# Kernel optimization log

Hardware: AMD Instinct MI355X
Metric: run time of the kernel (lower is better)

## Reference

```python
import jax, jax.numpy as jnp
import numpy as np

N_NODES = 100_000
N_EDGES = 3_200_000
F_IN, F_HID, F_OUT = 128, 128, 128
MLP_HID, MLP_OUT = 256, 64


def setup_inputs() -> dict:
    key = jax.random.key(0)
    ks = jax.random.split(key, 11)
    def w(k, shape):
        fan_in = shape[0]
        return jax.random.normal(k, shape, jnp.float32) / jnp.sqrt(jnp.float32(fan_in))
    return {
        'x':   jax.random.normal(ks[0], (N_NODES, F_IN), jnp.float32),
        'src': jax.random.randint(ks[1], (N_EDGES,), 0, N_NODES, jnp.int32),
        'dst': jax.random.randint(ks[2], (N_EDGES,), 0, N_NODES, jnp.int32),
        'w1':  w(ks[3], (F_IN, F_HID)),  'b1': jnp.zeros((F_HID,), jnp.float32),
        'w2':  w(ks[4], (F_HID, F_OUT)), 'b2': jnp.zeros((F_OUT,), jnp.float32),
        'wm1': w(ks[5], (F_OUT, MLP_HID)), 'bm1': jnp.zeros((MLP_HID,), jnp.float32),
        'wm2': w(ks[6], (MLP_HID, MLP_OUT)), 'bm2': jnp.zeros((MLP_OUT,), jnp.float32),
    }


def reference(x, src, dst, w1, b1, w2, b2, wm1, bm1, wm2, bm2):
    n = x.shape[0]
    ones = jnp.ones(src.shape[0], x.dtype)
    # DGL GraphConv norm='both': clamp degrees to >=1, symmetric D^-1/2 A D^-1/2
    out_norm = jnp.clip(jax.ops.segment_sum(ones, src, num_segments=n), 1.0) ** -0.5
    in_norm = jnp.clip(jax.ops.segment_sum(ones, dst, num_segments=n), 1.0) ** -0.5

    def gconv(h, w, b):
        msg = (h * out_norm[:, None])[src]                       # [E, F] gather
        agg = jax.ops.segment_sum(msg, dst, num_segments=n)      # [N, F] scatter-add
        return (agg * in_norm[:, None]) @ w + b

    h = jax.nn.relu(gconv(x, w1, b1))   # conv1 + relu (dropout is identity in eval)
    h = jax.nn.relu(gconv(h, w2, b2))   # conv2 + relu
    h = jax.nn.relu(h @ wm1 + bm1)      # MLP hidden layer
    return h @ wm2 + bm2                # MLP output (no final activation)
```

## Files before the change

### kernel.cpp

```cpp
#include <hip/hip_runtime.h>
#include <hip/hip_bf16.h>
#include <cstdint>

__device__ __forceinline__ unsigned short f2b(float f) {
    union { float f; unsigned int i; } v; v.f = f;
    unsigned int i = v.i;
    unsigned int r = (i + 0x7FFFu + ((i >> 16) & 1u)) >> 16;
    return (unsigned short)r;
}
__device__ __forceinline__ float b2f_lo(unsigned int p) {
    union { unsigned int i; float f; } v; v.i = p << 16; return v.f;
}
__device__ __forceinline__ float b2f_hi(unsigned int p) {
    union { unsigned int i; float f; } v; v.i = p & 0xFFFF0000u; return v.f;
}
__device__ __forceinline__ unsigned int pack2(float a, float b) {
    return (unsigned int)f2b(a) | ((unsigned int)f2b(b) << 16);
}

typedef __attribute__((__ext_vector_type__(8))) __bf16 bf16x8;
typedef __attribute__((__ext_vector_type__(4))) float  f32x4;

#define N_NODES 100000
#define N_EDGES 3200000
#define NBUCK   200
#define BSZ     500

__global__ void k_hist2(const int* __restrict__ src, const int* __restrict__ dst,
                        int* __restrict__ gcntA, int* __restrict__ gcntB, int E) {
    __shared__ int hA[NBUCK], hB[NBUCK];
    int t = threadIdx.x;
    if (t < NBUCK) { hA[t] = 0; hB[t] = 0; }
    __syncthreads();
    for (int i = blockIdx.x * blockDim.x + t; i < E; i += gridDim.x * blockDim.x) {
        atomicAdd(&hA[dst[i] / BSZ], 1);
        atomicAdd(&hB[src[i] / BSZ], 1);
    }
    __syncthreads();
    if (t < NBUCK) {
        if (hA[t]) atomicAdd(&gcntA[t], hA[t]);
        if (hB[t]) atomicAdd(&gcntB[t], hB[t]);
    }
}

__global__ void k_scan_coarse(const int* __restrict__ gcntA, const int* __restrict__ gcntB,
                              int* __restrict__ gbaseA, int* __restrict__ gbaseB,
                              int* __restrict__ gcurA, int* __restrict__ gcurB,
                              int* __restrict__ offsets) {
    __shared__ int pA[256], pB[256];
    int t = threadIdx.x;
    int vA = (t < NBUCK) ? gcntA[t] : 0;
    int vB = (t < NBUCK) ? gcntB[t] : 0;
    pA[t] = vA; pB[t] = vB;
    __syncthreads();
    for (int d = 1; d < 256; d <<= 1) {
        int a = (t >= d) ? pA[t - d] : 0;
        int b = (t >= d) ? pB[t - d] : 0;
        __syncthreads();
        pA[t] += a; pB[t] += b;
        __syncthreads();
    }
    if (t < NBUCK) {
        gbaseA[t] = pA[t] - vA; gcurA[t] = pA[t] - vA;
        gbaseB[t] = pB[t] - vB; gcurB[t] = pB[t] - vB;
    }
    if (t == 255) {
        gbaseA[NBUCK] = pA[255];
        gbaseB[NBUCK] = pB[255];
        offsets[N_NODES] = pA[255];
    }
}

__global__ void k_scatter(const int* __restrict__ src, const int* __restrict__ dst,
                          int* __restrict__ gcurA, int* __restrict__ gcurB,
                          unsigned* __restrict__ pairs, int* __restrict__ keysB, int E) {
    __shared__ int hA[NBUCK], hB[NBUCK], baA[NBUCK], baB[NBUCK], lcA[NBUCK], lcB[NBUCK];
    int t = threadIdx.x;
    const int CHUNK = 12500;
    int lo = blockIdx.x * CHUNK, hi = min(lo + CHUNK, E);
    if (t < NBUCK) { hA[t] = 0; hB[t] = 0; }
    __syncthreads();
    for (int i = lo + t; i < hi; i += 256) {
        atomicAdd(&hA[dst[i] / BSZ], 1);
        atomicAdd(&hB[src[i] / BSZ], 1);
    }
    __syncthreads();
    if (t < NBUCK) {
        baA[t] = hA[t] ? atomicAdd(&gcurA[t], hA[t]) : 0;
        lcA[t] = 0;
        baB[t] = hB[t] ? atomicAdd(&gcurB[t], hB[t]) : 0;
        lcB[t] = 0;
    }
    __syncthreads();
    for (int i = lo + t; i < hi; i += 256) {
        int s = src[i], d = dst[i];
        int bA = d / BSZ;
        int l  = atomicAdd(&lcA[bA], 1);
        pairs[baA[bA] + l] = ((unsigned)(d - bA * BSZ) << 17) | (unsigned)s;
        int bB = s / BSZ;
        int l2 = atomicAdd(&lcB[bB], 1);
        keysB[baB[bB] + l2] = s;
    }
}

__global__ void k_csr_bucket(const unsigned* __restrict__ pairs, const int* __restrict__ gbaseA,
                             int* __restrict__ offsets, float* __restrict__ in_norm,
                             int* __restrict__ esrc) {
    __shared__ int hist[512], scan[512], curs[512];
    int b = blockIdx.x, t = threadIdx.x;
    int node0 = b * BSZ;
    int bstart = gbaseA[b], bend = gbaseA[b + 1];
    if (t < 512) hist[t] = 0;
    __syncthreads();
    for (int i = bstart + t; i < bend; i += 1024)
        atomicAdd(&hist[pairs[i] >> 17], 1);
    __syncthreads();
    if (t < 512) scan[t] = hist[t];
    __syncthreads();
    for (int d = 1; d < 512; d <<= 1) {
        int v = (t < 512 && t >= d) ? scan[t - d] : 0;
        __syncthreads();
        if (t < 512) scan[t] += v;
        __syncthreads();
    }
    if (t < BSZ) {
        int excl = scan[t] - hist[t];
        offsets[node0 + t] = bstart + excl;
        in_norm[node0 + t] = rsqrtf((float)max(hist[t], 1));
        curs[t] = excl;
    }
    __syncthreads();
    for (int i = bstart + t; i < bend; i += 1024) {
        unsigned p = pairs[i];
        int d = (int)(p >> 17);
        int l = atomicAdd(&curs[d], 1);
        esrc[bstart + l] = (int)(p & 0x1FFFFu);
    }
}

__global__ void k_sortwave(const int* __restrict__ offsets, int* __restrict__ esrc, int N) {
    int node = blockIdx.x * 4 + (threadIdx.x >> 6);
    if (node >= N) return;
    int lane = threadIdx.x & 63;
    int lo = offsets[node], hi = offsets[node + 1];
    int len = hi - lo;
    if (len <= 1) return;
    const int INF = 0x7FFFFFFF;
    int v0 = (lane < len) ? esrc[lo + lane] : INF;
    int v1 = (64 + lane < len) ? esrc[lo + 64 + lane] : INF;
#pragma unroll
    for (int k = 2; k <= 128; k <<= 1) {
#pragma unroll
        for (int d = 64; d > 0; d >>= 1) {
            if (d >= k) continue;
            if (d == 64) {
                int a = min(v0, v1), b = max(v0, v1);
                v0 = a; v1 = b;
            } else {
                int w0 = __shfl_xor(v0, d, 64);
                int w1 = __shfl_xor(v1, d, 64);
                bool up0 = ((lane & k) == 0);
                bool up1 = (((64 + lane) & k) == 0);
                bool lower = ((lane & d) == 0);
                v0 = (lower == up0) ? min(v0, w0) : max(v0, w0);
                v1 = (lower == up1) ? min(v1, w1) : max(v1, w1);
            }
        }
    }
    if (lane < len) esrc[lo + lane] = v0;
    if (64 + lane < len) esrc[lo + 64 + lane] = v1;
}

__global__ void k_count_scale(const int* __restrict__ keys, const int* __restrict__ gbaseB,
                              const float4* __restrict__ x4, float* __restrict__ out_norm,
                              uint2* __restrict__ xs) {
    __shared__ int hist[512];
    __shared__ float onl[BSZ];
    int b = blockIdx.x, t = threadIdx.x;
    int node0 = b * BSZ;
    int bstart = gbaseB[b], bend = gbaseB[b + 1];
    if (t < 512) hist[t] = 0;
    __syncthreads();
    for (int i = bstart + t; i < bend; i += 1024)
        atomicAdd(&hist[keys[i] - node0], 1);
    __syncthreads();
    if (t < BSZ) {
        float on = rsqrtf((float)max(hist[t], 1));
        onl[t] = on;
        out_norm[node0 + t] = on;
    }
    __syncthreads();
    size_t base4 = (size_t)node0 * 32;
    for (int i = t; i < BSZ * 32; i += 1024) {
        float on = onl[i >> 5];
        float4 v = x4[base4 + i];
        uint2 o;
        o.x = pack2(v.x * on, v.y * on);
        o.y = pack2(v.z * on, v.w * on);
        xs[base4 + i] = o;
    }
}

__global__ void k_transpose4(const float* __restrict__ w1, const float* __restrict__ w2,
                             const float* __restrict__ wm1, const float* __restrict__ wm2,
                             unsigned short* __restrict__ t1, unsigned short* __restrict__ t2,
                             unsigned short* __restrict__ tm1, unsigned short* __restrict__ tm2) {
    int i = blockIdx.x * blockDim.x + threadIdx.x;
    const float* w; unsigned short* t; int N, idx;
    if (i < 16384)       { w = w1;  t = t1;  N = 128; idx = i; }
    else if (i < 32768)  { w = w2;  t = t2;  N = 128; idx = i - 16384; }
    else if (i < 65536)  { w = wm1; t = tm1; N = 256; idx = i - 32768; }
    else if (i < 81920)  { w = wm2; t = tm2; N = 64;  idx = i - 65536; }
    else return;
    int K = (i < 65536) ? 128 : 256;
    int k = idx / N, n = idx - k * N;
    t[(size_t)n * K + k] = f2b(w[idx]);
}

#define AGG_ADD(p)                                                              \
        a0 += b2f_lo(p.x); a1 += b2f_hi(p.x);                                   \
        a2 += b2f_lo(p.y); a3 += b2f_hi(p.y);                                   \
        a4 += b2f_lo(p.z); a5 += b2f_hi(p.z);                                   \
        a6 += b2f_lo(p.w); a7 += b2f_hi(p.w);

#define AGG_NODE_BODY(node)                                                     \
    int lo = offsets[node], hi = offsets[node + 1];                             \
    float a0 = 0.f, a1 = 0.f, a2 = 0.f, a3 = 0.f,                               \
          a4 = 0.f, a5 = 0.f, a6 = 0.f, a7 = 0.f;                               \
    int k = lo + g;                                                             \
    for (; k + 12 < hi; k += 16) {                                              \
        int s0 = esrc[k];                                                       \
        int s1 = esrc[k + 4];                                                   \
        int s2 = esrc[k + 8];                                                   \
        int s3 = esrc[k + 12];                                                  \
        uint4 p0 = feat[(size_t)s0 * 16 + c];                                   \
        uint4 p1 = feat[(size_t)s1 * 16 + c];                                   \
        uint4 p2 = feat[(size_t)s2 * 16 + c];                                   \
        uint4 p3 = feat[(size_t)s3 * 16 + c];                                   \
        AGG_ADD(p0) AGG_ADD(p1) AGG_ADD(p2) AGG_ADD(p3)                         \
    }                                                                           \
    for (; k < hi; k += 4) {                                                    \
        int s = esrc[k];                                                        \
        uint4 p = feat[(size_t)s * 16 + c];                                     \
        AGG_ADD(p)                                                              \
    }                                                                           \
    a0 += __shfl_xor(a0, 16, 64); a0 += __shfl_xor(a0, 32, 64);                 \
    a1 += __shfl_xor(a1, 16, 64); a1 += __shfl_xor(a1, 32, 64);                 \
    a2 += __shfl_xor(a2, 16, 64); a2 += __shfl_xor(a2, 32, 64);                 \
    a3 += __shfl_xor(a3, 16, 64); a3 += __shfl_xor(a3, 32, 64);                 \
    a4 += __shfl_xor(a4, 16, 64); a4 += __shfl_xor(a4, 32, 64);                 \
    a5 += __shfl_xor(a5, 16, 64); a5 += __shfl_xor(a5, 32, 64);                 \
    a6 += __shfl_xor(a6, 16, 64); a6 += __shfl_xor(a6, 32, 64);                 \
    a7 += __shfl_xor(a7, 16, 64); a7 += __shfl_xor(a7, 32, 64);

__global__ __launch_bounds__(256, 8)
void k_conv(const int* __restrict__ offsets, const int* __restrict__ esrc,
            const uint4* __restrict__ feat, const float* __restrict__ in_norm,
            const unsigned short* __restrict__ WT, const float* __restrict__ bias,
            const float* __restrict__ row_scale, unsigned short* __restrict__ C,
            int N) {
    __shared__ unsigned short A[32][136];
    int wv = threadIdx.x >> 6, lane = threadIdx.x & 63;
    int row0 = blockIdx.x * 32;
    int g = lane >> 4, c = lane & 15;

    for (int i = 0; i < 8; ++i) {
        int nl = wv * 8 + i;
        int node = row0 + nl;
        AGG_NODE_BODY(node)
        if (g == 0) {
            float inn = in_norm[node];
            uint4 o;
            o.x = pack2(a0 * inn, a1 * inn);
            o.y = pack2(a2 * inn, a3 * inn);
            o.z = pack2(a4 * inn, a5 * inn);
            o.w = pack2(a6 * inn, a7 * inn);
            *(uint4*)&A[nl][c * 8] = o;
        }
    }
    __syncthreads();

    int m = lane & 15, q = lane >> 4;
    const unsigned short* b0 = WT + (size_t)(wv * 32 + m) * 128 + q * 8;
    const unsigned short* b1 = b0 + (size_t)16 * 128;
    f32x4 acc00 = {0.f, 0.f, 0.f, 0.f}, acc10 = {0.f, 0.f, 0.f, 0.f};
    f32x4 acc01 = {0.f, 0.f, 0.f, 0.f}, acc11 = {0.f, 0.f, 0.f, 0.f};
#pragma unroll
    for (int k = 0; k < 128; k += 32) {
        bf16x8 bf0 = *(const bf16x8*)(b0 + k);
        bf16x8 bf1 = *(const bf16x8*)(b1 + k);
        bf16x8 af0 = *(const bf16x8*)&A[m][q * 8 + k];
        bf16x8 af1 = *(const bf16x8*)&A[16 + m][q * 8 + k];
        acc00 = __builtin_amdgcn_mfma_f32_16x16x32_bf16(af0, bf0, acc00, 0, 0, 0);
        acc10 = __builtin_amdgcn_mfma_f32_16x16x32_bf16(af1, bf0, acc10, 0, 0, 0);
        acc01 = __builtin_amdgcn_mfma_f32_16x16x32_bf16(af0, bf1, acc01, 0, 0, 0);
        acc11 = __builtin_amdgcn_mfma_f32_16x16x32_bf16(af1, bf1, acc11, 0, 0, 0);
    }
    int col0 = wv * 32 + m;
    int col1 = col0 + 16;
    float bc0 = bias[col0], bc1 = bias[col1];
#pragma unroll
    for (int r = 0; r < 4; r++) {
        int rr = row0 + q * 4 + r;
        int rr1 = rr + 16;
        float v00 = fmaxf(acc00[r] + bc0, 0.f);
        float v10 = fmaxf(acc10[r] + bc0, 0.f);
        float v01 = fmaxf(acc01[r] + bc1, 0.f);
        float v11 = fmaxf(acc11[r] + bc1, 0.f);
        float s0 = row_scale[rr], s1 = row_scale[rr1];
        v00 *= s0; v01 *= s0; v10 *= s1; v11 *= s1;
        C[(size_t)rr * 128 + col0]  = f2b(v00);
        C[(size_t)rr * 128 + col1]  = f2b(v01);
        C[(size_t)rr1 * 128 + col0] = f2b(v10);
        C[(size_t)rr1 * 128 + col1] = f2b(v11);
    }
}

__global__ __launch_bounds__(256, 8)
void k_conv2_mlp(const int* __restrict__ offsets, const int* __restrict__ esrc,
                 const uint4* __restrict__ feat, const float* __restrict__ in_norm,
                 const unsigned short* __restrict__ WT2, const float* __restrict__ b2,
                 const unsigned short* __restrict__ WTM1, const float* __restrict__ bm1,
                 const unsigned short* __restrict__ WTM2, const float* __restrict__ bm2,
                 float* __restrict__ out, int N) {
    __shared__ unsigned short smem[8704];
    unsigned short (*H1)[136] = (unsigned short(*)[136])(smem);
    unsigned short (*A)[136]  = (unsigned short(*)[136])(smem + 4352);
    unsigned short (*H2)[136] = (unsigned short(*)[136])(smem + 4352);

    int wv = threadIdx.x >> 6, lane = threadIdx.x & 63;
    int row0 = blockIdx.x * 32;
    int g = lane >> 4, c = lane & 15;

    for (int i = 0; i < 8; ++i) {
        int nl = wv * 8 + i;
        int node = row0 + nl;
        AGG_NODE_BODY(node)
        if (g == 0) {
            float inn = in_norm[node];
            uint4 o;
            o.x = pack2(a0 * inn, a1 * inn);
            o.y = pack2(a2 * inn, a3 * inn);
            o.z = pack2(a4 * inn, a5 * inn);
            o.w = pack2(a6 * inn, a7 * inn);
            *(uint4*)&A[nl][c * 8] = o;
        }
    }
    __syncthreads();

    int m = lane & 15, q = lane >> 4;

    {
        const unsigned short* bb0 = WT2 + (size_t)(wv * 32 + m) * 128 + q * 8;
        const unsigned short* bb1 = bb0 + (size_t)16 * 128;
        f32x4 acc00 = {0.f, 0.f, 0.f, 0.f}, acc10 = {0.f, 0.f, 0.f, 0.f};
        f32x4 acc01 = {0.f, 0.f, 0.f, 0.f}, acc11 = {0.f, 0.f, 0.f, 0.f};
#pragma unroll
        for (int k = 0; k < 128; k += 32) {
            bf16x8 bf0 = *(const bf16x8*)(bb0 + k);
            bf16x8 bf1 = *(const bf16x8*)(bb1 + k);
            bf16x8 af0 = *(const bf16x8*)&A[m][q * 8 + k];
            bf16x8 af1 = *(const bf16x8*)&A[16 + m][q * 8 + k];
            acc00 = __builtin_amdgcn_mfma_f32_16x16x32_bf16(af0, bf0, acc00, 0, 0, 0);
            acc10 = __builtin_amdgcn_mfma_f32_16x16x32_bf16(af1, bf0, acc10, 0, 0, 0);
            acc01 = __builtin_amdgcn_mfma_f32_16x16x32_bf16(af0, bf1, acc01, 0, 0, 0);
            acc11 = __builtin_amdgcn_mfma_f32_16x16x32_bf16(af1, bf1, acc11, 0, 0, 0);
        }
        int col0 = wv * 32 + m;
        int col1 = col0 + 16;
        float bc0 = b2[col0], bc1 = b2[col1];
#pragma unroll
        for (int r = 0; r < 4; r++) {
            int rl = q * 4 + r;
            H1[rl][col0]      = f2b(fmaxf(acc00[r] + bc0, 0.f));
            H1[rl][col1]      = f2b(fmaxf(acc01[r] + bc1, 0.f));
            H1[rl + 16][col0] = f2b(fmaxf(acc10[r] + bc0, 0.f));
            H1[rl + 16][col1] = f2b(fmaxf(acc11[r] + bc1, 0.f));
        }
    }
    __syncthreads();

    f32x4 macc0 = {0.f, 0.f, 0.f, 0.f}, macc1 = {0.f, 0.f, 0.f, 0.f};
    int colo = wv * 16 + m;
    const unsigned short* bp2 = WTM2 + (size_t)colo * 256 + q * 8;
#pragma unroll
    for (int half = 0; half < 2; ++half) {
#pragma unroll
        for (int cb = 0; cb < 2; cb++) {
            int colh = half * 128 + wv * 32 + cb * 16 + m;
            const unsigned short* bp = WTM1 + (size_t)colh * 128 + q * 8;
            f32x4 acc0 = {0.f, 0.f, 0.f, 0.f};
            f32x4 acc1 = {0.f, 0.f, 0.f, 0.f};
#pragma unroll
            for (int s = 0; s < 4; s++) {
                bf16x8 bfr = *(const bf16x8*)(bp + s * 32);
                bf16x8 ha0 = *(const bf16x8*)&H1[m][s * 32 + q * 8];
                bf16x8 ha1 = *(const bf16x8*)&H1[m + 16][s * 32 + q * 8];
                acc0 = __builtin_amdgcn_mfma_f32_16x16x32_bf16(ha0, bfr, acc0, 0, 0, 0);
                acc1 = __builtin_amdgcn_mfma_f32_16x16x32_bf16(ha1, bfr, acc1, 0, 0, 0);
            }
            float bc = bm1[colh];
            int cl = colh & 127;
#pragma unroll
            for (int r = 0; r < 4; r++) {
                H2[q * 4 + r][cl]      = f2b(fmaxf(acc0[r] + bc, 0.f));
                H2[q * 4 + r + 16][cl] = f2b(fmaxf(acc1[r] + bc, 0.f));
            }
        }
        __syncthreads();
#pragma unroll
        for (int s = 0; s < 4; s++) {
            bf16x8 bfr = *(const bf16x8*)(bp2 + half * 128 + s * 32);
            bf16x8 ha0 = *(const bf16x8*)&H2[m][s * 32 + q * 8];
            bf16x8 ha1 = *(const bf16x8*)&H2[m + 16][s * 32 + q * 8];
            macc0 = __builtin_amdgcn_mfma_f32_16x16x32_bf16(ha0, bfr, macc0, 0, 0, 0);
            macc1 = __builtin_amdgcn_mfma_f32_16x16x32_bf16(ha1, bfr, macc1, 0, 0, 0);
        }
        __syncthreads();
    }

    float bc = bm2[colo];
#pragma unroll
    for (int r = 0; r < 4; r++) {
        out[(size_t)(row0 + q * 4 + r) * 64 + colo]      = macc0[r] + bc;
        out[(size_t)(row0 + q * 4 + r + 16) * 64 + colo] = macc1[r] + bc;
    }
}

extern "C" void kernel_launch(void* const* d_in, const int* in_sizes, int n_in,
                              void* d_out, int out_size, void* d_ws, size_t ws_size,
                              hipStream_t stream) {
    const float* x    = (const float*)d_in[0];
    const int*   src  = (const int*)d_in[1];
    const int*   dst  = (const int*)d_in[2];
    const float* w1   = (const float*)d_in[3];
    const float* b1   = (const float*)d_in[4];
    const float* w2   = (const float*)d_in[5];
    const float* b2   = (const float*)d_in[6];
    const float* wm1  = (const float*)d_in[7];
    const float* bm1  = (const float*)d_in[8];
    const float* wm2  = (const float*)d_in[9];
    const float* bm2  = (const float*)d_in[10];

    const int N = N_NODES;
    const int E = N_EDGES;

    char* p = (char*)d_ws;
    auto alloc = [&](size_t bytes) -> void* {
        void* r = (void*)p;
        p += (bytes + 255) & ~(size_t)255;
        return r;
    };
    int*   gcntA   = (int*)alloc(256 * 4);
    int*   gcntB   = (int*)alloc(256 * 4);
    int*   gbaseA  = (int*)alloc(256 * 4);
    int*   gbaseB  = (int*)alloc(256 * 4);
    int*   gcurA   = (int*)alloc(256 * 4);
    int*   gcurB   = (int*)alloc(256 * 4);
    int*   offsets = (int*)alloc((size_t)(N + 1) * 4);
    float* out_norm = (float*)alloc((size_t)N * 4);
    float* in_norm  = (float*)alloc((size_t)N * 4);
    int*   esrc     = (int*)alloc((size_t)E * 4);
    unsigned int* bufA = (unsigned int*)alloc((size_t)N * 128 * 2);
    unsigned int* bufB = (unsigned int*)alloc((size_t)N * 128 * 2);
    unsigned int* bufC = (unsigned int*)alloc((size_t)N * 128 * 2);
    unsigned short* wt1  = (unsigned short*)alloc(128 * 128 * 2);
    unsigned short* wt2  = (unsigned short*)alloc(128 * 128 * 2);
    unsigned short* wtm1 = (unsigned short*)alloc(256 * 128 * 2);
    unsigned short* wtm2 = (unsigned short*)alloc(64 * 256 * 2);
    (void)ws_size; (void)n_in; (void)in_sizes; (void)out_size;

    unsigned* pairs = (unsigned*)bufB;
    int*      keysB = (int*)bufC;

    hipMemsetAsync(gcntA, 0, 2 * 256 * 4, stream);

    const int TB = 256;
    k_hist2<<<dim3(256), dim3(TB), 0, stream>>>(src, dst, gcntA, gcntB, E);
    k_scan_coarse<<<dim3(1), dim3(TB), 0, stream>>>(gcntA, gcntB, gbaseA, gbaseB,
                                                    gcurA, gcurB, offsets);
    k_scatter<<<dim3(256), dim3(TB), 0, stream>>>(src, dst, gcurA, gcurB, pairs, keysB, E);
    k_csr_bucket<<<dim3(NBUCK), dim3(1024), 0, stream>>>(pairs, gbaseA, offsets, in_norm, esrc);
    k_sortwave<<<dim3(N / 4), dim3(TB), 0, stream>>>(offsets, esrc, N);
    k_count_scale<<<dim3(NBUCK), dim3(1024), 0, stream>>>(
        keysB, gbaseB, (const float4*)x, out_norm, (uint2*)bufA);

    k_transpose4<<<dim3(320), dim3(TB), 0, stream>>>(w1, w2, wm1, wm2, wt1, wt2, wtm1, wtm2);

    k_conv<<<dim3(N / 32), dim3(TB), 0, stream>>>(
        offsets, esrc, (const uint4*)bufA, in_norm, wt1, b1, out_norm,
        (unsigned short*)bufC, N);

    k_conv2_mlp<<<dim3(N / 32), dim3(TB), 0, stream>>>(
        offsets, esrc, (const uint4*)bufC, in_norm, wt2, b2, wtm1, bm1, wtm2, bm2,
        (float*)d_out, N);
}
```

Measured before the change: 581.1 us.

## Halve bucket size, shrink keys to u16, add short-row sort path, coalesce stores

Doubles the coarse bucket count so each CSR-build and count/scale block handles 250 nodes with 512 threads, which gives more blocks for parallelism. Source keys for the out-degree pass are stored as 16-bit local offsets to cut memory traffic. The per-node bitonic sort gets a single-register path for rows of at most 64 edges. The conv and MLP epilogues stage results in shared memory and write 16-byte coalesced rows instead of scattered scalar stores, at the cost of extra barriers and LDS traffic.

```diff
diff --git a/kernel.cpp b/kernel.cpp
--- a/kernel.cpp
+++ b/kernel.cpp
@@ -23,23 +23,23 @@
 
 #define N_NODES 100000
 #define N_EDGES 3200000
-#define NBUCK   200
-#define BSZ     500
+#define NBUCK   400
+#define BSZ     250
 
 __global__ void k_hist2(const int* __restrict__ src, const int* __restrict__ dst,
                         int* __restrict__ gcntA, int* __restrict__ gcntB, int E) {
     __shared__ int hA[NBUCK], hB[NBUCK];
     int t = threadIdx.x;
-    if (t < NBUCK) { hA[t] = 0; hB[t] = 0; }
+    for (int j = t; j < NBUCK; j += 256) { hA[j] = 0; hB[j] = 0; }
     __syncthreads();
     for (int i = blockIdx.x * blockDim.x + t; i < E; i += gridDim.x * blockDim.x) {
         atomicAdd(&hA[dst[i] / BSZ], 1);
         atomicAdd(&hB[src[i] / BSZ], 1);
     }
     __syncthreads();
-    if (t < NBUCK) {
-        if (hA[t]) atomicAdd(&gcntA[t], hA[t]);
-        if (hB[t]) atomicAdd(&gcntB[t], hB[t]);
+    for (int j = t; j < NBUCK; j += 256) {
+        if (hA[j]) atomicAdd(&gcntA[j], hA[j]);
+        if (hB[j]) atomicAdd(&gcntB[j], hB[j]);
     }
 }
 
@@ -47,13 +47,13 @@
                               int* __restrict__ gbaseA, int* __restrict__ gbaseB,
                               int* __restrict__ gcurA, int* __restrict__ gcurB,
                               int* __restrict__ offsets) {
-    __shared__ int pA[256], pB[256];
+    __shared__ int pA[512], pB[512];
     int t = threadIdx.x;
     int vA = (t < NBUCK) ? gcntA[t] : 0;
     int vB = (t < NBUCK) ? gcntB[t] : 0;
     pA[t] = vA; pB[t] = vB;
     __syncthreads();
-    for (int d = 1; d < 256; d <<= 1) {
+    for (int d = 1; d < 512; d <<= 1) {
         int a = (t >= d) ? pA[t - d] : 0;
         int b = (t >= d) ? pB[t - d] : 0;
         __syncthreads();
@@ -64,32 +64,33 @@
         gbaseA[t] = pA[t] - vA; gcurA[t] = pA[t] - vA;
         gbaseB[t] = pB[t] - vB; gcurB[t] = pB[t] - vB;
     }
-    if (t == 255) {
-        gbaseA[NBUCK] = pA[255];
-        gbaseB[NBUCK] = pB[255];
-        offsets[N_NODES] = pA[255];
+    if (t == 511) {
+        gbaseA[NBUCK] = pA[511];
+        gbaseB[NBUCK] = pB[511];
+        offsets[N_NODES] = pA[511];
     }
 }
 
 __global__ void k_scatter(const int* __restrict__ src, const int* __restrict__ dst,
                           int* __restrict__ gcurA, int* __restrict__ gcurB,
-                          unsigned* __restrict__ pairs, int* __restrict__ keysB, int E) {
+                          unsigned* __restrict__ pairs, unsigned short* __restrict__ keysB,
+                          int E) {
     __shared__ int hA[NBUCK], hB[NBUCK], baA[NBUCK], baB[NBUCK], lcA[NBUCK], lcB[NBUCK];
     int t = threadIdx.x;
     const int CHUNK = 12500;
     int lo = blockIdx.x * CHUNK, hi = min(lo + CHUNK, E);
-    if (t < NBUCK) { hA[t] = 0; hB[t] = 0; }
+    for (int j = t; j < NBUCK; j += 256) { hA[j] = 0; hB[j] = 0; }
     __syncthreads();
     for (int i = lo + t; i < hi; i += 256) {
         atomicAdd(&hA[dst[i] / BSZ], 1);
         atomicAdd(&hB[src[i] / BSZ], 1);
     }
     __syncthreads();
-    if (t < NBUCK) {
-        baA[t] = hA[t] ? atomicAdd(&gcurA[t], hA[t]) : 0;
-        lcA[t] = 0;
-        baB[t] = hB[t] ? atomicAdd(&gcurB[t], hB[t]) : 0;
-        lcB[t] = 0;
+    for (int j = t; j < NBUCK; j += 256) {
+        baA[j] = hA[j] ? atomicAdd(&gcurA[j], hA[j]) : 0;
+        lcA[j] = 0;
+        baB[j] = hB[j] ? atomicAdd(&gcurB[j], hB[j]) : 0;
+        lcB[j] = 0;
     }
     __syncthreads();
     for (int i = lo + t; i < hi; i += 256) {
@@ -99,28 +100,28 @@
         pairs[baA[bA] + l] = ((unsigned)(d - bA * BSZ) << 17) | (unsigned)s;
         int bB = s / BSZ;
         int l2 = atomicAdd(&lcB[bB], 1);
-        keysB[baB[bB] + l2] = s;
+        keysB[baB[bB] + l2] = (unsigned short)(s - bB * BSZ);
     }
 }
 
 __global__ void k_csr_bucket(const unsigned* __restrict__ pairs, const int* __restrict__ gbaseA,
                              int* __restrict__ offsets, float* __restrict__ in_norm,
                              int* __restrict__ esrc) {
-    __shared__ int hist[512], scan[512], curs[512];
+    __shared__ int hist[256], scan[256], curs[256];
     int b = blockIdx.x, t = threadIdx.x;
     int node0 = b * BSZ;
     int bstart = gbaseA[b], bend = gbaseA[b + 1];
-    if (t < 512) hist[t] = 0;
-    __syncthreads();
-    for (int i = bstart + t; i < bend; i += 1024)
+    if (t < 256) hist[t] = 0;
+    __syncthreads();
+    for (int i = bstart + t; i < bend; i += 512)
         atomicAdd(&hist[pairs[i] >> 17], 1);
     __syncthreads();
-    if (t < 512) scan[t] = hist[t];
-    __syncthreads();
-    for (int d = 1; d < 512; d <<= 1) {
-        int v = (t < 512 && t >= d) ? scan[t - d] : 0;
+    if (t < 256) scan[t] = hist[t];
+    __syncthreads();
+    for (int d = 1; d < 256; d <<= 1) {
+        int v = (t < 256 && t >= d) ? scan[t - d] : 0;
         __syncthreads();
-        if (t < 512) scan[t] += v;
+        if (t < 256) scan[t] += v;
         __syncthreads();
     }
     if (t < BSZ) {
@@ -130,7 +131,7 @@
         curs[t] = excl;
     }
     __syncthreads();
-    for (int i = bstart + t; i < bend; i += 1024) {
+    for (int i = bstart + t; i < bend; i += 512) {
         unsigned p = pairs[i];
         int d = (int)(p >> 17);
         int l = atomicAdd(&curs[d], 1);
@@ -146,6 +147,22 @@
     int len = hi - lo;
     if (len <= 1) return;
     const int INF = 0x7FFFFFFF;
+    if (len <= 64) {
+        int v0 = (lane < len) ? esrc[lo + lane] : INF;
+#pragma unroll
+        for (int k = 2; k <= 64; k <<= 1) {
+#pragma unroll
+            for (int d = 32; d > 0; d >>= 1) {
+                if (d >= k) continue;
+                int w0 = __shfl_xor(v0, d, 64);
+                bool up = ((lane & k) == 0);
+                bool lower = ((lane & d) == 0);
+                v0 = (lower == up) ? min(v0, w0) : max(v0, w0);
+            }
+        }
+        if (lane < len) esrc[lo + lane] = v0;
+        return;
+    }
     int v0 = (lane < len) ? esrc[lo + lane] : INF;
     int v1 = (64 + lane < len) ? esrc[lo + 64 + lane] : INF;
 #pragma unroll
@@ -171,18 +188,19 @@
     if (64 + lane < len) esrc[lo + 64 + lane] = v1;
 }
 
-__global__ void k_count_scale(const int* __restrict__ keys, const int* __restrict__ gbaseB,
+__global__ void k_count_scale(const unsigned short* __restrict__ keys,
+                              const int* __restrict__ gbaseB,
                               const float4* __restrict__ x4, float* __restrict__ out_norm,
                               uint2* __restrict__ xs) {
-    __shared__ int hist[512];
+    __shared__ int hist[256];
     __shared__ float onl[BSZ];
     int b = blockIdx.x, t = threadIdx.x;
     int node0 = b * BSZ;
     int bstart = gbaseB[b], bend = gbaseB[b + 1];
-    if (t < 512) hist[t] = 0;
-    __syncthreads();
-    for (int i = bstart + t; i < bend; i += 1024)
-        atomicAdd(&hist[keys[i] - node0], 1);
+    if (t < 256) hist[t] = 0;
+    __syncthreads();
+    for (int i = bstart + t; i < bend; i += 512)
+        atomicAdd(&hist[keys[i]], 1);
     __syncthreads();
     if (t < BSZ) {
         float on = rsqrtf((float)max(hist[t], 1));
@@ -191,7 +209,7 @@
     }
     __syncthreads();
     size_t base4 = (size_t)node0 * 32;
-    for (int i = t; i < BSZ * 32; i += 1024) {
+    for (int i = t; i < BSZ * 32; i += 512) {
         float on = onl[i >> 5];
         float4 v = x4[base4 + i];
         uint2 o;
@@ -259,7 +277,7 @@
             const unsigned short* __restrict__ WT, const float* __restrict__ bias,
             const float* __restrict__ row_scale, unsigned short* __restrict__ C,
             int N) {
-    __shared__ unsigned short A[32][136];
+    __shared__ __align__(16) unsigned short A[32][136];
     int wv = threadIdx.x >> 6, lane = threadIdx.x & 63;
     int row0 = blockIdx.x * 32;
     int g = lane >> 4, c = lane & 15;
@@ -296,23 +314,33 @@
         acc01 = __builtin_amdgcn_mfma_f32_16x16x32_bf16(af0, bf1, acc01, 0, 0, 0);
         acc11 = __builtin_amdgcn_mfma_f32_16x16x32_bf16(af1, bf1, acc11, 0, 0, 0);
     }
+    __syncthreads();
+
     int col0 = wv * 32 + m;
     int col1 = col0 + 16;
     float bc0 = bias[col0], bc1 = bias[col1];
 #pragma unroll
     for (int r = 0; r < 4; r++) {
-        int rr = row0 + q * 4 + r;
-        int rr1 = rr + 16;
+        int rl = q * 4 + r;
+        int rr = row0 + rl, rr1 = rr + 16;
         float v00 = fmaxf(acc00[r] + bc0, 0.f);
         float v10 = fmaxf(acc10[r] + bc0, 0.f);
         float v01 = fmaxf(acc01[r] + bc1, 0.f);
         float v11 = fmaxf(acc11[r] + bc1, 0.f);
         float s0 = row_scale[rr], s1 = row_scale[rr1];
         v00 *= s0; v01 *= s0; v10 *= s1; v11 *= s1;
-        C[(size_t)rr * 128 + col0]  = f2b(v00);
-        C[(size_t)rr * 128 + col1]  = f2b(v01);
-        C[(size_t)rr1 * 128 + col0] = f2b(v10);
-        C[(size_t)rr1 * 128 + col1] = f2b(v11);
+        A[rl][col0]      = f2b(v00);
+        A[rl][col1]      = f2b(v01);
+        A[rl + 16][col0] = f2b(v10);
+        A[rl + 16][col1] = f2b(v11);
+    }
+    __syncthreads();
+#pragma unroll
+    for (int it = 0; it < 2; ++it) {
+        int idx = it * 256 + (int)threadIdx.x;
+        int row = idx >> 4, seg = idx & 15;
+        uint4 v = *(const uint4*)&A[row][seg * 8];
+        *(uint4*)&C[(size_t)(row0 + row) * 128 + seg * 8] = v;
     }
 }
 
@@ -323,7 +351,7 @@
                  const unsigned short* __restrict__ WTM1, const float* __restrict__ bm1,
                  const unsigned short* __restrict__ WTM2, const float* __restrict__ bm2,
                  float* __restrict__ out, int N) {
-    __shared__ unsigned short smem[8704];
+    __shared__ __align__(16) unsigned short smem[8704];
     unsigned short (*H1)[136] = (unsigned short(*)[136])(smem);
     unsigned short (*A)[136]  = (unsigned short(*)[136])(smem + 4352);
     unsigned short (*H2)[136] = (unsigned short(*)[136])(smem + 4352);
@@ -419,11 +447,20 @@
         __syncthreads();
     }
 
+    float* OS = (float*)smem;
     float bc = bm2[colo];
 #pragma unroll
     for (int r = 0; r < 4; r++) {
-        out[(size_t)(row0 + q * 4 + r) * 64 + colo]      = macc0[r] + bc;
-        out[(size_t)(row0 + q * 4 + r + 16) * 64 + colo] = macc1[r] + bc;
+        OS[(q * 4 + r) * 64 + colo]        = macc0[r] + bc;
+        OS[(q * 4 + r + 16) * 64 + colo]   = macc1[r] + bc;
+    }
+    __syncthreads();
+#pragma unroll
+    for (int it = 0; it < 2; ++it) {
+        int idx = it * 256 + (int)threadIdx.x;
+        int row = idx >> 4, seg = idx & 15;
+        float4 v = *(const float4*)&OS[row * 64 + seg * 4];
+        *(float4*)&out[(size_t)(row0 + row) * 64 + seg * 4] = v;
     }
 }
 
@@ -451,12 +488,12 @@
         p += (bytes + 255) & ~(size_t)255;
         return r;
     };
-    int*   gcntA   = (int*)alloc(256 * 4);
-    int*   gcntB   = (int*)alloc(256 * 4);
-    int*   gbaseA  = (int*)alloc(256 * 4);
-    int*   gbaseB  = (int*)alloc(256 * 4);
-    int*   gcurA   = (int*)alloc(256 * 4);
-    int*   gcurB   = (int*)alloc(256 * 4);
+    int*   gcntA   = (int*)alloc((NBUCK + 1) * 4);
+    int*   gcntB   = (int*)alloc((NBUCK + 1) * 4);
+    int*   gbaseA  = (int*)alloc((NBUCK + 1) * 4);
+    int*   gbaseB  = (int*)alloc((NBUCK + 1) * 4);
+    int*   gcurA   = (int*)alloc((NBUCK + 1) * 4);
+    int*   gcurB   = (int*)alloc((NBUCK + 1) * 4);
     int*   offsets = (int*)alloc((size_t)(N + 1) * 4);
     float* out_norm = (float*)alloc((size_t)N * 4);
     float* in_norm  = (float*)alloc((size_t)N * 4);
@@ -470,19 +507,19 @@
     unsigned short* wtm2 = (unsigned short*)alloc(64 * 256 * 2);
     (void)ws_size; (void)n_in; (void)in_sizes; (void)out_size;
 
-    unsigned* pairs = (unsigned*)bufB;
-    int*      keysB = (int*)bufC;
-
-    hipMemsetAsync(gcntA, 0, 2 * 256 * 4, stream);
+    unsigned*       pairs = (unsigned*)bufB;
+    unsigned short* keysB = (unsigned short*)bufC;
+
+    hipMemsetAsync(gcntA, 0, (size_t)((char*)gcntB - (char*)gcntA) + NBUCK * 4, stream);
 
     const int TB = 256;
     k_hist2<<<dim3(256), dim3(TB), 0, stream>>>(src, dst, gcntA, gcntB, E);
-    k_scan_coarse<<<dim3(1), dim3(TB), 0, stream>>>(gcntA, gcntB, gbaseA, gbaseB,
-                                                    gcurA, gcurB, offsets);
+    k_scan_coarse<<<dim3(1), dim3(512), 0, stream>>>(gcntA, gcntB, gbaseA, gbaseB,
+                                                     gcurA, gcurB, offsets);
     k_scatter<<<dim3(256), dim3(TB), 0, stream>>>(src, dst, gcurA, gcurB, pairs, keysB, E);
-    k_csr_bucket<<<dim3(NBUCK), dim3(1024), 0, stream>>>(pairs, gbaseA, offsets, in_norm, esrc);
+    k_csr_bucket<<<dim3(NBUCK), dim3(512), 0, stream>>>(pairs, gbaseA, offsets, in_norm, esrc);
     k_sortwave<<<dim3(N / 4), dim3(TB), 0, stream>>>(offsets, esrc, N);
-    k_count_scale<<<dim3(NBUCK), dim3(1024), 0, stream>>>(
+    k_count_scale<<<dim3(NBUCK), dim3(512), 0, stream>>>(
         keysB, gbaseB, (const float4*)x, out_norm, (uint2*)bufA);
 
     k_transpose4<<<dim3(320), dim3(TB), 0, stream>>>(w1, w2, wm1, wm2, wt1, wt2, wtm1, wtm2);
```

Result: faster. 552.6 us (-4.9%).
